# Kernel tuning notes

Hardware: AMD Instinct MI355X
Metric: run time of the kernel (lower is better)

## Reference

```python
import jax, jax.numpy as jnp
import numpy as np

EPS = 1e-5

def _conv(x, w, pad):
    # NCHW / OIHW 2-D convolution, stride 1
    return jax.lax.conv_general_dilated(
        x, w, window_strides=(1, 1), padding=[(pad, pad), (pad, pad)],
        dimension_numbers=('NCHW', 'OIHW', 'NCHW'))

def _bn2d(x, g, b, m, v):
    inv = g * jax.lax.rsqrt(v + EPS)
    return x * inv[None, :, None, None] + (b - m * inv)[None, :, None, None]

def _bn1d(x, g, b, m, v):
    inv = g * jax.lax.rsqrt(v + EPS)
    return x * inv[None, :] + (b - m * inv)[None, :]

def _avgpool2(x):
    B, C, H, W = x.shape
    return x.reshape(B, C, H // 2, 2, W // 2, 2).mean(axis=(3, 5))

def _hardtanh01(x):
    return jnp.clip(x, 0.0, 1.0)

def setup_inputs() -> dict:
    key = jax.random.key(0)
    ks = jax.random.split(key, 24)
    B = 1024
    d = {}
    d['x_in'] = jax.random.normal(ks[0], (B, 3, 32, 32), dtype=jnp.float32)
    d['w1'] = jax.random.normal(ks[1], (32, 3, 5, 5), dtype=jnp.float32) * 0.1
    d['w2'] = jax.random.normal(ks[2], (32, 32, 5, 5), dtype=jnp.float32) * 0.05
    d['w3'] = jax.random.normal(ks[3], (64, 32, 5, 5), dtype=jnp.float32) * 0.05
    d['w4'] = jax.random.normal(ks[4], (10, 64, 4, 4), dtype=jnp.float32) * 0.05
    for i, (c, k0) in enumerate([(32, 5), (32, 9), (64, 13), (10, 17)], start=1):
        d[f'g{i}'] = jax.random.uniform(ks[k0], (c,), minval=0.5, maxval=1.5, dtype=jnp.float32)
        d[f'b{i}'] = jax.random.normal(ks[k0 + 1], (c,), dtype=jnp.float32) * 0.1
        d[f'm{i}'] = jax.random.normal(ks[k0 + 2], (c,), dtype=jnp.float32) * 0.1
        d[f'v{i}'] = jax.random.uniform(ks[k0 + 3], (c,), minval=0.5, maxval=1.5, dtype=jnp.float32)
    return d

def reference(x_in, w1, w2, w3, w4,
              g1, b1, m1, v1, g2, b2, m2, v2,
              g3, b3, m3, v3, g4, b4, m4, v4):
    # conv1 -> bn1 -> pool -> hardtanh(0,1)
    x = _hardtanh01(_avgpool2(_bn2d(_conv(x_in, w1, 2), g1, b1, m1, v1)))
    # conv2 -> bn2 -> pool -> hardtanh(0,1)
    x = _hardtanh01(_avgpool2(_bn2d(_conv(x, w2, 2), g2, b2, m2, v2)))
    # conv3 -> bn3 -> pool -> hardtanh(0,1)
    x = _hardtanh01(_avgpool2(_bn2d(_conv(x, w3, 2), g3, b3, m3, v3)))
    # fc1 as 4x4 conv, valid padding -> (B, num_classes, 1, 1)
    x = _conv(x, w4, 0).reshape(x.shape[0], -1)
    return _bn1d(x, g4, b4, m4, v4)
```

## Files before the change

### kernel.cpp

```cpp
#include <hip/hip_runtime.h>

#define EPSF 1e-5f

typedef _Float16 half8 __attribute__((ext_vector_type(8)));
typedef _Float16 half4v __attribute__((ext_vector_type(4)));
typedef float f32x4 __attribute__((ext_vector_type(4)));

__device__ __forceinline__ float clamp01(float x){ return fminf(fmaxf(x, 0.f), 1.f); }

__global__ __launch_bounds__(256) void k_prep(
    const float* __restrict__ w1, const float* __restrict__ w2,
    const float* __restrict__ w3, const float* __restrict__ w4,
    const float* __restrict__ g1, const float* __restrict__ b1, const float* __restrict__ m1, const float* __restrict__ v1,
    const float* __restrict__ g2, const float* __restrict__ b2, const float* __restrict__ m2, const float* __restrict__ v2,
    const float* __restrict__ g3, const float* __restrict__ b3, const float* __restrict__ m3, const float* __restrict__ v3,
    const float* __restrict__ g4, const float* __restrict__ b4, const float* __restrict__ m4, const float* __restrict__ v4,
    _Float16* __restrict__ w1h, _Float16* __restrict__ w2h, _Float16* __restrict__ w3h,
    _Float16* __restrict__ w4h, float* __restrict__ bnc)
{
  const int t = blockIdx.x*256 + threadIdx.x;
  if (t < 5120) {
    int oc = t / 160, k = t - oc*160;
    int dy = k >> 5, rem = k & 31, dx = rem >> 2, ic = rem & 3;
    float val = (dx < 5 && ic < 3) ? w1[(oc*3+ic)*25 + dy*5 + dx] : 0.f;
    w1h[t] = (_Float16)val;
  }
  for (int i = t; i < 25600; i += 32768) {
    int tap = i >> 10, r = i & 1023, oc = r >> 5, ic = r & 31;
    w2h[i] = (_Float16)w2[(oc*32+ic)*25 + tap];
  }
  for (int i = t; i < 51200; i += 32768) {
    int tap = i >> 11, r = i & 2047, oc = r >> 5, ic = r & 31;
    w3h[i] = (_Float16)w3[(oc*32+ic)*25 + tap];
  }
  for (int i = t; i < 16384; i += 32768) {
    int oc = i >> 10, k = i & 1023, pos = k >> 6, ic = k & 63;
    float val = (oc < 10) ? w4[(oc*64+ic)*16 + pos] : 0.f;
    w4h[i] = (_Float16)val;
  }
  if (t < 32) {
    float inv = g1[t] / sqrtf(v1[t] + EPSF);
    bnc[t] = 0.25f*inv; bnc[32+t] = b1[t] - m1[t]*inv;
    float i2 = g2[t] / sqrtf(v2[t] + EPSF);
    bnc[64+t] = 0.25f*i2; bnc[96+t] = b2[t] - m2[t]*i2;
  }
  if (t < 64) {
    float i3 = g3[t] / sqrtf(v3[t] + EPSF);
    bnc[128+t] = 0.25f*i3; bnc[192+t] = b3[t] - m3[t]*i3;
  }
  if (t < 10) {
    float i4 = g4[t] / sqrtf(v4[t] + EPSF);
    bnc[256+t] = i4; bnc[266+t] = b4[t] - m4[t]*i4;
  }
}

__global__ __launch_bounds__(256, 4) void k_fused(
    const float* __restrict__ x,
    const _Float16* __restrict__ w1h, const _Float16* __restrict__ w2h,
    const _Float16* __restrict__ w3h, const _Float16* __restrict__ w4h,
    const float* __restrict__ bnc, float* __restrict__ out)
{
  __shared__ __align__(16) char arena[32000];
  _Float16* Bx1 = (_Float16*)arena;
  _Float16* P2  = (_Float16*)arena;
  _Float16* P3  = (_Float16*)arena;
  _Float16* Ip3 = (_Float16*)(arena + 11520);
  float*    S4P = (float*)(arena + 13568);

  const int img = blockIdx.x;
  const int tid = threadIdx.x;
  const int w   = __builtin_amdgcn_readfirstlane(tid >> 6);
  const int l   = tid & 63;
  const int row = l & 15;
  const int kg  = l >> 4;

  {
    const float* xin = x + img*3072;
    for (int j = tid; j < 1330; j += 256) {
      int y = j / 38, xx = j - y*38;
      float s0 = 0.f, s1 = 0.f, s2 = 0.f;
      #pragma unroll
      for (int r = 0; r < 2; ++r) {
        int iy = y - 2 + r;
        if ((unsigned)iy < 32u) {
          #pragma unroll
          for (int c = 0; c < 2; ++c) {
            int ix = xx - 2 + c;
            if ((unsigned)ix < 32u) {
              int o = iy*32 + ix;
              s0 += xin[o]; s1 += xin[1024 + o]; s2 += xin[2048 + o];
            }
          }
        }
      }
      half4v h; h[0] = (_Float16)s0; h[1] = (_Float16)s1; h[2] = (_Float16)s2; h[3] = (_Float16)0.f;
      *(half4v*)(Bx1 + y*160 + xx*4) = h;
    }
  }
  __syncthreads();

  f32x4 acc1[4][2];
  {
    half8 B1[5][2];
    #pragma unroll
    for (int dy = 0; dy < 5; ++dy) {
      B1[dy][0] = *(const half8*)(w1h + row*160 + dy*32 + kg*8);
      B1[dy][1] = *(const half8*)(w1h + (16 + row)*160 + dy*32 + kg*8);
    }
    #pragma unroll
    for (int mt = 0; mt < 4; ++mt) { acc1[mt][0] = (f32x4){0,0,0,0}; acc1[mt][1] = (f32x4){0,0,0,0}; }
    const int xoff = 8*(row + kg);
    #pragma unroll
    for (int mt = 0; mt < 4; ++mt) {
      const int py = w*4 + mt;
      #pragma unroll
      for (int dy = 0; dy < 5; ++dy) {
        half8 av = *(const half8*)(Bx1 + (2*py + dy)*160 + xoff);
        acc1[mt][0] = __builtin_amdgcn_mfma_f32_16x16x32_f16(av, B1[dy][0], acc1[mt][0], 0, 0, 0);
        acc1[mt][1] = __builtin_amdgcn_mfma_f32_16x16x32_f16(av, B1[dy][1], acc1[mt][1], 0, 0, 0);
      }
    }
  }
  __syncthreads();

  for (int j = tid; j < 1600; j += 256) {
    int u = j & 3, pos = j >> 2;
    int a = pos/20, c = pos - a*20;
    bool interior = ((unsigned)(a-2) < 16u) & ((unsigned)(c-2) < 16u);
    if (!interior) *(half8*)(P2 + pos*40 + u*8) = (half8)(_Float16)0.f;
  }
  {
    const float s0 = bnc[row],      h0 = bnc[32 + row];
    const float s1 = bnc[16 + row], h1 = bnc[48 + row];
    #pragma unroll
    for (int mt = 0; mt < 4; ++mt) {
      const int py = w*4 + mt;
      #pragma unroll
      for (int r = 0; r < 4; ++r) {
        int pcol = kg*4 + r;
        int idx = ((py+2)*20 + pcol+2)*40;
        P2[idx + row]      = (_Float16)clamp01(fmaf(acc1[mt][0][r], s0, h0));
        P2[idx + 16 + row] = (_Float16)clamp01(fmaf(acc1[mt][1][r], s1, h1));
      }
    }
  }
  __syncthreads();

  f32x4 a2_0 = {0,0,0,0}, a2_1 = {0,0,0,0};
  {
    const int pixel = w*16 + row;
    const int py = pixel >> 3, px = pixel & 7;
    const _Float16* base = P2 + ((2*py)*20 + 2*px)*40 + kg*8;
    half8 RA[6], RB[6];
    #pragma unroll
    for (int c = 0; c < 6; ++c) RA[c] = *(const half8*)(base + c*40);
    #pragma unroll
    for (int c = 0; c < 6; ++c) RB[c] = *(const half8*)(base + 800 + c*40);
    const _Float16* wb = w2h + row*32 + kg*8;
    half8 cw0 = *(const half8*)(wb);
    half8 cw1 = *(const half8*)(wb + 512);
    #pragma unroll
    for (int dy = 0; dy < 5; ++dy) {
      half8 cs[6];
      #pragma unroll
      for (int c = 0; c < 6; ++c) cs[c] = RA[c] + RB[c];
      if (dy < 4) {
        #pragma unroll
        for (int c = 0; c < 6; ++c) {
          half8 nv = *(const half8*)(base + (dy+2)*800 + c*40);
          if ((dy & 1) == 0) RA[c] = nv; else RB[c] = nv;
        }
      }
      #pragma unroll
      for (int dx = 0; dx < 5; ++dx) {
        const int tap = dy*5 + dx;
        const int tn = (tap < 24) ? tap + 1 : 24;
        half8 nw0 = *(const half8*)(wb + tn*1024);
        half8 nw1 = *(const half8*)(wb + tn*1024 + 512);
        half8 av = cs[dx] + cs[dx+1];
        a2_0 = __builtin_amdgcn_mfma_f32_16x16x32_f16(av, cw0, a2_0, 0, 0, 0);
        a2_1 = __builtin_amdgcn_mfma_f32_16x16x32_f16(av, cw1, a2_1, 0, 0, 0);
        cw0 = nw0; cw1 = nw1;
      }
    }
  }
  __syncthreads();

  for (int j = tid; j < 576; j += 256) {
    int u = j & 3, pos = j >> 2;
    int a = pos/12, c = pos - a*12;
    bool interior = ((unsigned)(a-2) < 8u) & ((unsigned)(c-2) < 8u);
    if (!interior) *(half8*)(P3 + pos*40 + u*8) = (half8)(_Float16)0.f;
  }
  {
    const float s0 = bnc[64 + row], h0 = bnc[96 + row];
    const float s1 = bnc[80 + row], h1 = bnc[112 + row];
    #pragma unroll
    for (int r = 0; r < 4; ++r) {
      int p2 = w*16 + kg*4 + r;
      int py2 = p2 >> 3, px2 = p2 & 7;
      int idx = ((py2+2)*12 + px2+2)*40;
      P3[idx + row]      = (_Float16)clamp01(fmaf(a2_0[r], s0, h0));
      P3[idx + 16 + row] = (_Float16)clamp01(fmaf(a2_1[r], s1, h1));
    }
  }
  __syncthreads();

  {
    const int py = row >> 2, px = row & 3;
    const _Float16* base = P3 + ((2*py)*12 + 2*px)*40 + kg*8;
    half8 RA[6], RB[6];
    #pragma unroll
    for (int c = 0; c < 6; ++c) RA[c] = *(const half8*)(base + c*40);
    #pragma unroll
    for (int c = 0; c < 6; ++c) RB[c] = *(const half8*)(base + 480 + c*40);
    const _Float16* wb = w3h + (w*16 + row)*32 + kg*8;
    half8 cw = *(const half8*)(wb);
    f32x4 a3 = {0,0,0,0};
    #pragma unroll
    for (int dy = 0; dy < 5; ++dy) {
      half8 cs[6];
      #pragma unroll
      for (int c = 0; c < 6; ++c) cs[c] = RA[c] + RB[c];
      if (dy < 4) {
        #pragma unroll
        for (int c = 0; c < 6; ++c) {
          half8 nv = *(const half8*)(base + (dy+2)*480 + c*40);
          if ((dy & 1) == 0) RA[c] = nv; else RB[c] = nv;
        }
      }
      #pragma unroll
      for (int dx = 0; dx < 5; ++dx) {
        const int tap = dy*5 + dx;
        const int tn = (tap < 24) ? tap + 1 : 24;
        half8 nw = *(const half8*)(wb + tn*2048);
        half8 av = cs[dx] + cs[dx+1];
        a3 = __builtin_amdgcn_mfma_f32_16x16x32_f16(av, cw, a3, 0, 0, 0);
        cw = nw;
      }
    }
    const int oc = w*16 + row;
    const float s3 = bnc[128 + oc], h3 = bnc[192 + oc];
    #pragma unroll
    for (int r = 0; r < 4; ++r)
      Ip3[(kg*4 + r)*64 + oc] = (_Float16)clamp01(fmaf(a3[r], s3, h3));
  }
  __syncthreads();

  if (tid < 160) {
    const int oc = tid >> 4, pix = tid & 15;
    const _Float16* A = Ip3 + pix*64;
    const _Float16* W = w4h + oc*1024 + pix*64;
    float a = 0.f;
    #pragma unroll
    for (int q = 0; q < 8; ++q) {
      half8 xa = *(const half8*)(A + q*8);
      half8 wv = *(const half8*)(W + q*8);
      #pragma unroll
      for (int j = 0; j < 8; ++j)
        a = fmaf((float)xa[j], (float)wv[j], a);
    }
    S4P[tid] = a;
  }
  __syncthreads();
  if (tid < 10) {
    float s = 0.f;
    #pragma unroll
    for (int i = 0; i < 16; ++i) s += S4P[tid*16 + i];
    out[img*10 + tid] = fmaf(s, bnc[256 + tid], bnc[266 + tid]);
  }
}

extern "C" void kernel_launch(void* const* d_in, const int* in_sizes, int n_in,
                              void* d_out, int out_size, void* d_ws, size_t ws_size,
                              hipStream_t stream)
{
  const float* x  = (const float*)d_in[0];
  const float* w1 = (const float*)d_in[1];
  const float* w2 = (const float*)d_in[2];
  const float* w3 = (const float*)d_in[3];
  const float* w4 = (const float*)d_in[4];
  const float *g1=(const float*)d_in[5],  *b1=(const float*)d_in[6],
              *m1=(const float*)d_in[7],  *v1=(const float*)d_in[8];
  const float *g2=(const float*)d_in[9],  *b2=(const float*)d_in[10],
              *m2=(const float*)d_in[11], *v2=(const float*)d_in[12];
  const float *g3=(const float*)d_in[13], *b3=(const float*)d_in[14],
              *m3=(const float*)d_in[15], *v3=(const float*)d_in[16];
  const float *g4=(const float*)d_in[17], *b4=(const float*)d_in[18],
              *m4=(const float*)d_in[19], *v4=(const float*)d_in[20];
  float* out = (float*)d_out;

  char* ws = (char*)d_ws;
  _Float16* w1h = (_Float16*)(ws);
  _Float16* w2h = (_Float16*)(ws + 10240);
  _Float16* w3h = (_Float16*)(ws + 61440);
  _Float16* w4h = (_Float16*)(ws + 163840);
  float*    bnc = (float*)   (ws + 196608);

  k_prep<<<dim3(128), dim3(256), 0, stream>>>(w1, w2, w3, w4,
      g1,b1,m1,v1, g2,b2,m2,v2, g3,b3,m3,v3, g4,b4,m4,v4,
      w1h, w2h, w3h, w4h, bnc);
  k_fused<<<dim3(1024), dim3(256), 0, stream>>>(x, w1h, w2h, w3h, w4h, bnc, out);
}
```

Before: 129.9 us.

## Stage input image in LDS and interleave channels for paired half2 stores

Loads the whole input image into shared memory with coalesced float4 loads before building the box-summed conv1 input, replacing uncoalesced repeated global reads. It also permutes output-channel order in the conv1/conv2 weight prep so each lane owns two adjacent channels and writes them as a single half2 LDS store. This cuts global memory traffic and LDS store count, but adds an extra barrier and 12KB of LDS usage during the first phase.

New measurement: 126.9 us. -2.3%, faster.

```diff
diff --git a/kernel.cpp b/kernel.cpp
--- a/kernel.cpp
+++ b/kernel.cpp
@@ -4,6 +4,7 @@
 
 typedef _Float16 half8 __attribute__((ext_vector_type(8)));
 typedef _Float16 half4v __attribute__((ext_vector_type(4)));
+typedef _Float16 half2v __attribute__((ext_vector_type(2)));
 typedef float f32x4 __attribute__((ext_vector_type(4)));
 
 __device__ __forceinline__ float clamp01(float x){ return fminf(fmaxf(x, 0.f), 1.f); }
@@ -20,13 +21,15 @@
 {
   const int t = blockIdx.x*256 + threadIdx.x;
   if (t < 5120) {
-    int oc = t / 160, k = t - oc*160;
+    int c = t / 160, k = t - c*160;
+    int oc = (c < 16) ? 2*c : 2*(c-16)+1;
     int dy = k >> 5, rem = k & 31, dx = rem >> 2, ic = rem & 3;
     float val = (dx < 5 && ic < 3) ? w1[(oc*3+ic)*25 + dy*5 + dx] : 0.f;
     w1h[t] = (_Float16)val;
   }
   for (int i = t; i < 25600; i += 32768) {
-    int tap = i >> 10, r = i & 1023, oc = r >> 5, ic = r & 31;
+    int tap = i >> 10, r = i & 1023, c = r >> 5, ic = r & 31;
+    int oc = (c < 16) ? 2*c : 2*(c-16)+1;
     w2h[i] = (_Float16)w2[(oc*32+ic)*25 + tap];
   }
   for (int i = t; i < 51200; i += 32768) {
@@ -62,6 +65,7 @@
 {
   __shared__ __align__(16) char arena[32000];
   _Float16* Bx1 = (_Float16*)arena;
+  float*    Img = (float*)(arena + 11264);
   _Float16* P2  = (_Float16*)arena;
   _Float16* P3  = (_Float16*)arena;
   _Float16* Ip3 = (_Float16*)(arena + 11520);
@@ -75,27 +79,31 @@
   const int kg  = l >> 4;
 
   {
-    const float* xin = x + img*3072;
-    for (int j = tid; j < 1330; j += 256) {
-      int y = j / 38, xx = j - y*38;
-      float s0 = 0.f, s1 = 0.f, s2 = 0.f;
-      #pragma unroll
-      for (int r = 0; r < 2; ++r) {
-        int iy = y - 2 + r;
-        if ((unsigned)iy < 32u) {
-          #pragma unroll
-          for (int c = 0; c < 2; ++c) {
-            int ix = xx - 2 + c;
-            if ((unsigned)ix < 32u) {
-              int o = iy*32 + ix;
-              s0 += xin[o]; s1 += xin[1024 + o]; s2 += xin[2048 + o];
-            }
+    const float4* src = (const float4*)(x + img*3072);
+    float4* dst = (float4*)Img;
+    dst[tid] = src[tid]; dst[tid+256] = src[tid+256]; dst[tid+512] = src[tid+512];
+  }
+  __syncthreads();
+
+  for (int j = tid; j < 1400; j += 256) {
+    int y = j / 40, xx = j - y*40;
+    float s0 = 0.f, s1 = 0.f, s2 = 0.f;
+    #pragma unroll
+    for (int r = 0; r < 2; ++r) {
+      int iy = y - 2 + r;
+      if ((unsigned)iy < 32u) {
+        #pragma unroll
+        for (int cc = 0; cc < 2; ++cc) {
+          int ix = xx - 2 + cc;
+          if ((unsigned)ix < 32u) {
+            const float* ip = Img + iy*32 + ix;
+            s0 += ip[0]; s1 += ip[1024]; s2 += ip[2048];
           }
         }
       }
-      half4v h; h[0] = (_Float16)s0; h[1] = (_Float16)s1; h[2] = (_Float16)s2; h[3] = (_Float16)0.f;
-      *(half4v*)(Bx1 + y*160 + xx*4) = h;
-    }
+    }
+    half4v h; h[0] = (_Float16)s0; h[1] = (_Float16)s1; h[2] = (_Float16)s2; h[3] = (_Float16)0.f;
+    *(half4v*)(Bx1 + y*160 + xx*4) = h;
   }
   __syncthreads();
 
@@ -130,8 +138,9 @@
     if (!interior) *(half8*)(P2 + pos*40 + u*8) = (half8)(_Float16)0.f;
   }
   {
-    const float s0 = bnc[row],      h0 = bnc[32 + row];
-    const float s1 = bnc[16 + row], h1 = bnc[48 + row];
+    const int oce = 2*row;
+    const float sA = bnc[oce],   hA = bnc[32 + oce];
+    const float sB = bnc[oce+1], hB = bnc[32 + oce + 1];
     #pragma unroll
     for (int mt = 0; mt < 4; ++mt) {
       const int py = w*4 + mt;
@@ -139,8 +148,10 @@
       for (int r = 0; r < 4; ++r) {
         int pcol = kg*4 + r;
         int idx = ((py+2)*20 + pcol+2)*40;
-        P2[idx + row]      = (_Float16)clamp01(fmaf(acc1[mt][0][r], s0, h0));
-        P2[idx + 16 + row] = (_Float16)clamp01(fmaf(acc1[mt][1][r], s1, h1));
+        half2v h;
+        h[0] = (_Float16)clamp01(fmaf(acc1[mt][0][r], sA, hA));
+        h[1] = (_Float16)clamp01(fmaf(acc1[mt][1][r], sB, hB));
+        *(half2v*)(P2 + idx + oce) = h;
       }
     }
   }
@@ -193,15 +204,18 @@
     if (!interior) *(half8*)(P3 + pos*40 + u*8) = (half8)(_Float16)0.f;
   }
   {
-    const float s0 = bnc[64 + row], h0 = bnc[96 + row];
-    const float s1 = bnc[80 + row], h1 = bnc[112 + row];
+    const int oce = 2*row;
+    const float sA = bnc[64 + oce],   hA = bnc[96 + oce];
+    const float sB = bnc[64 + oce+1], hB = bnc[96 + oce + 1];
     #pragma unroll
     for (int r = 0; r < 4; ++r) {
       int p2 = w*16 + kg*4 + r;
       int py2 = p2 >> 3, px2 = p2 & 7;
       int idx = ((py2+2)*12 + px2+2)*40;
-      P3[idx + row]      = (_Float16)clamp01(fmaf(a2_0[r], s0, h0));
-      P3[idx + 16 + row] = (_Float16)clamp01(fmaf(a2_1[r], s1, h1));
+      half2v h;
+      h[0] = (_Float16)clamp01(fmaf(a2_0[r], sA, hA));
+      h[1] = (_Float16)clamp01(fmaf(a2_1[r], sB, hB));
+      *(half2v*)(P3 + idx + oce) = h;
     }
   }
   __syncthreads();
```
